# Performance work log

Measured on AMD Instinct MI355X. Metric: run time of the kernel, lower is better.

## Reference

```python
import jax, jax.numpy as jnp
import numpy as np

B, S, D, H = 4, 2048, 1024, 16
DEPTH = D // H  # 64


def setup_inputs() -> dict:
    key = jax.random.key(0)
    ks = jax.random.split(key, 11)
    scale = 1.0 / np.sqrt(D)
    inp = {
        "v": jax.random.normal(ks[0], (B, S, D), jnp.float32),
        "k": jax.random.normal(ks[1], (B, S, D), jnp.float32),
        "q": jax.random.normal(ks[2], (B, S, D), jnp.float32),
        # causal mask: 1.0 where attention is disallowed (strict upper triangle)
        "mask": jnp.triu(jnp.ones((S, S), jnp.float32), k=1)[None, None, :, :],
        "wq": jax.random.normal(ks[3], (D, D), jnp.float32) * scale,
        "bq": jnp.zeros((D,), jnp.float32),
        "wk": jax.random.normal(ks[4], (D, D), jnp.float32) * scale,
        "bk": jnp.zeros((D,), jnp.float32),
        "wv": jax.random.normal(ks[5], (D, D), jnp.float32) * scale,
        "bv": jnp.zeros((D,), jnp.float32),
        "wo": jax.random.normal(ks[6], (D, D), jnp.float32) * scale,
        "bo": jnp.zeros((D,), jnp.float32),
    }
    return inp


def _split_heads(x):
    # [B, S, D] -> [B, H, S, depth]
    b, s, _ = x.shape
    return x.reshape(b, s, H, DEPTH).transpose(0, 2, 1, 3)


def reference(v, k, q, mask, wq, bq, wk, bk, wv, bv, wo, bo):
    qh = _split_heads(q @ wq + bq)  # [B,H,S,depth]
    kh = _split_heads(k @ wk + bk)
    vh = _split_heads(v @ wv + bv)

    logits = jnp.einsum("bhqd,bhkd->bhqk", qh, kh) / jnp.sqrt(
        jnp.asarray(DEPTH, jnp.float32)
    )
    logits = logits + mask * -1e9
    attn = jax.nn.softmax(logits, axis=-1)  # [B,H,S,S]
    out = jnp.einsum("bhqk,bhkd->bhqd", attn, vh)
    out = out.transpose(0, 2, 1, 3).reshape(q.shape[0], -1, D)  # [B,S,D]
    return out @ wo + bo
```

## Files before the change

### kernel.cpp

```cpp
#include <hip/hip_runtime.h>

typedef _Float16 f16;
typedef _Float16 half8 __attribute__((ext_vector_type(8)));
typedef _Float16 half4v __attribute__((ext_vector_type(4)));
typedef _Float16 half2v __attribute__((ext_vector_type(2)));
typedef float f32x4 __attribute__((ext_vector_type(4)));

__device__ __forceinline__ void gl_lds16(const void* g, void* l) {
    __builtin_amdgcn_global_load_lds((const __attribute__((address_space(1))) void*)g,
                                     (__attribute__((address_space(3))) void*)l, 16, 0, 0);
}

__device__ __forceinline__ unsigned pack_f16(float a, float b) {
    union { half2v h; unsigned u; } un;
    un.h[0] = (f16)a; un.h[1] = (f16)b;
    return un.u;
}

__device__ __forceinline__ void prep_w_body(const float* __restrict__ W, f16* __restrict__ Wt)
{
    __shared__ float t[64][65];
    const int tid = threadIdx.x;
    const int tk = blockIdx.x * 64, tn = blockIdx.y * 64;
    const int rr = tid >> 4, cc = (tid & 15) * 4;
    #pragma unroll
    for (int j = 0; j < 4; ++j) {
        float4 v = *(const float4*)(W + (size_t)(tk + rr + j * 16) * 1024 + tn + cc);
        t[rr + j * 16][cc] = v.x; t[rr + j * 16][cc + 1] = v.y;
        t[rr + j * 16][cc + 2] = v.z; t[rr + j * 16][cc + 3] = v.w;
    }
    __syncthreads();
    const int n = tid >> 2, kc = (tid & 3) * 16;
    f16 o[16];
    #pragma unroll
    for (int j = 0; j < 16; ++j) o[j] = (f16)t[kc + j][n];
    f16* dst = Wt + (size_t)(tn + n) * 1024 + tk + kc;
    *(uint4*)dst = *(uint4*)o;
    *(uint4*)(dst + 8) = *(uint4*)(o + 8);
}

__global__ __launch_bounds__(256) void prep_w1(const float* __restrict__ W, f16* __restrict__ Wt)
{ prep_w_body(W, Wt); }

__global__ __launch_bounds__(256) void prep_w3(const float* __restrict__ w0,
    const float* __restrict__ w1, const float* __restrict__ w2, f16* __restrict__ Wt)
{
    const int z = blockIdx.z;
    const float* W = (z == 0) ? w0 : (z == 1) ? w1 : w2;
    prep_w_body(W, Wt + (size_t)z * 1024 * 1024);
}

__global__ __launch_bounds__(512, 4) void qkv_gemm(
    const float* __restrict__ Xq, const float* __restrict__ Xk, const float* __restrict__ Xv,
    const f16* __restrict__ Wt,
    const float* __restrict__ bqp, const float* __restrict__ bkp, const float* __restrict__ bvp,
    f16* __restrict__ qh, f16* __restrict__ kh, f16* __restrict__ vth)
{
    __shared__ __align__(16) f16 As[2][128 * 32];
    __shared__ __align__(16) f16 Bs[2][256 * 32];

    const int z = blockIdx.z;
    const float* X    = (z == 0) ? Xq : (z == 1) ? Xk : Xv;
    const float* bias = (z == 0) ? bqp : (z == 1) ? bkp : bvp;
    const f16*   W    = Wt + (size_t)z * 1024 * 1024;

    const int tid = threadIdx.x;
    const int lane = tid & 63;
    const int lane16 = lane & 15, quad = lane >> 4;
    const int l2 = lane16 & 3;
    const int wave = tid >> 6;
    const int wm = (wave & 1) * 64;
    const int wn = (wave >> 1) * 64;

    const int lin = blockIdx.x + 4 * blockIdx.y;
    const int xcd = lin & 7, t = lin >> 3;
    const int m0 = (((t >> 2) << 3) | xcd) * 128;
    const int n0 = (t & 3) * 256;

    const int xrow = tid >> 2, xch = tid & 3;
    const size_t xgbase = (size_t)(m0 + xrow) * 1024 + xch * 8;
    f16* const pA0 = As[0] + xrow * 32 + ((xch ^ (xrow & 3)) * 8);
    f16* const pA1 = As[1] + xrow * 32 + ((xch ^ (xrow & 3)) * 8);

    const int wrow0 = tid >> 2;
    const int wch = tid & 3;
    const size_t wg0 = (size_t)(n0 + wrow0) * 1024 + ((wch ^ (wrow0 & 3)) * 8);
    const size_t wg1 = (size_t)(n0 + 128 + wrow0) * 1024 + ((wch ^ (wrow0 & 3)) * 8);
    const int wldsbase = (tid & 448) * 8;

    f32x4 acc[4][4] = {};

    {
        float4 x0 = *(const float4*)(X + xgbase);
        float4 x1 = *(const float4*)(X + xgbase + 4);
        gl_lds16(W + wg0, Bs[0] + wldsbase);
        gl_lds16(W + wg1, Bs[0] + 4096 + wldsbase);
        asm volatile("s_waitcnt vmcnt(2)" ::: "memory");
        half8 hx;
        hx[0] = (f16)x0.x; hx[1] = (f16)x0.y; hx[2] = (f16)x0.z; hx[3] = (f16)x0.w;
        hx[4] = (f16)x1.x; hx[5] = (f16)x1.y; hx[6] = (f16)x1.z; hx[7] = (f16)x1.w;
        *(half8*)pA0 = hx;
        asm volatile("s_waitcnt vmcnt(0) lgkmcnt(0)" ::: "memory");
        __builtin_amdgcn_s_barrier();
        asm volatile("" ::: "memory");
    }

    for (int kt = 0; kt < 32; ++kt) {
        const int cur = kt & 1;
        const bool pf = (kt + 1 < 32);
        const f16* Ab = As[cur];
        const f16* Bb = Bs[cur];

        float4 x0, x1;
        if (pf) {
            const int k1 = (kt + 1) * 32;
            x0 = *(const float4*)(X + xgbase + k1);
            x1 = *(const float4*)(X + xgbase + k1 + 4);
            gl_lds16(W + wg0 + k1, Bs[cur ^ 1] + wldsbase);
            gl_lds16(W + wg1 + k1, Bs[cur ^ 1] + 4096 + wldsbase);
        }

        half8 af[4], bf[4];
        #pragma unroll
        for (int i = 0; i < 4; ++i)
            af[i] = *(const half8*)(Ab + (wm + i * 16 + lane16) * 32 + ((quad ^ l2) * 8));
        #pragma unroll
        for (int i = 0; i < 4; ++i)
            bf[i] = *(const half8*)(Bb + (wn + i * 16 + lane16) * 32 + ((quad ^ l2) * 8));
        #pragma unroll
        for (int mi = 0; mi < 4; ++mi)
            #pragma unroll
            for (int ni = 0; ni < 4; ++ni)
                acc[mi][ni] = __builtin_amdgcn_mfma_f32_16x16x32_f16(af[mi], bf[ni], acc[mi][ni], 0, 0, 0);

        if (pf) {
            asm volatile("s_waitcnt vmcnt(2)" ::: "memory");
            half8 hx;
            hx[0] = (f16)x0.x; hx[1] = (f16)x0.y; hx[2] = (f16)x0.z; hx[3] = (f16)x0.w;
            hx[4] = (f16)x1.x; hx[5] = (f16)x1.y; hx[6] = (f16)x1.z; hx[7] = (f16)x1.w;
            *(half8*)((cur == 1) ? pA0 : pA1) = hx;
        }
        asm volatile("s_waitcnt vmcnt(0) lgkmcnt(0)" ::: "memory");
        __builtin_amdgcn_s_barrier();
        asm volatile("" ::: "memory");
    }

    #pragma unroll
    for (int mi = 0; mi < 4; ++mi) {
        #pragma unroll
        for (int ni = 0; ni < 4; ++ni) {
            const int col = n0 + wn + ni * 16 + lane16;
            const float bval = bias[col];
            const int grow0 = m0 + wm + mi * 16 + quad * 4;
            if (z == 2) {
                const int b = grow0 >> 11, s0 = grow0 & 2047;
                const int h = col >> 6, d = col & 63;
                half4v p;
                #pragma unroll
                for (int r = 0; r < 4; ++r) p[r] = (f16)(acc[mi][ni][r] + bval);
                *(half4v*)(vth + (((size_t)b * 16 + h) * 64 + d) * 2048 + s0) = p;
            } else {
                f16* out = (z == 0) ? qh : kh;
                #pragma unroll
                for (int r = 0; r < 4; ++r)
                    out[(size_t)(grow0 + r) * 1024 + col] = (f16)(acc[mi][ni][r] + bval);
            }
        }
    }
}

__global__ __launch_bounds__(256, 2) void out_gemm(
    const f16* __restrict__ X, const f16* __restrict__ Wt,
    const float* __restrict__ bias, float* __restrict__ out)
{
    __shared__ __align__(16) f16 As[2][128 * 64];
    __shared__ __align__(16) f16 Bs[2][128 * 64];

    const int tid = threadIdx.x;
    const int lane = tid & 63;
    const int lane16 = lane & 15, quad = lane >> 4;
    const int wave = tid >> 6;
    const int wm = (wave >> 1) * 64, wn = (wave & 1) * 64;

    const int lin = blockIdx.x + 8 * blockIdx.y;
    const int xcd = lin & 7, t = lin >> 3;
    const int m0 = ((t >> 3) * 8 + xcd) * 128;
    const int n0 = (t & 7) * 128;

    const int wbase = tid & 192;
    const int srow = tid >> 3, schunk = tid & 7;
    const int swc = schunk ^ (srow & 7);

    f32x4 acc[4][4] = {};

    #pragma unroll
    for (int i = 0; i < 4; ++i) {
        gl_lds16(Wt + (size_t)(n0 + i * 32 + srow) * 1024 + swc * 8, Bs[0] + (size_t)(i * 256 + wbase) * 8);
        gl_lds16(X  + (size_t)(m0 + i * 32 + srow) * 1024 + swc * 8, As[0] + (size_t)(i * 256 + wbase) * 8);
    }

    for (int kt = 0; kt < 16; ++kt) {
        if (kt + 1 < 16) {
            const int nb = (kt + 1) & 1;
            const int k1 = (kt + 1) * 64;
            #pragma unroll
            for (int i = 0; i < 4; ++i) {
                gl_lds16(Wt + (size_t)(n0 + i * 32 + srow) * 1024 + k1 + swc * 8, Bs[nb] + (size_t)(i * 256 + wbase) * 8);
                gl_lds16(X  + (size_t)(m0 + i * 32 + srow) * 1024 + k1 + swc * 8, As[nb] + (size_t)(i * 256 + wbase) * 8);
            }
            asm volatile("s_waitcnt vmcnt(8)" ::: "memory");
        } else {
            asm volatile("s_waitcnt vmcnt(0)" ::: "memory");
        }
        __builtin_amdgcn_s_barrier();
        asm volatile("" ::: "memory");

        const f16* Ab = As[kt & 1];
        const f16* Bb = Bs[kt & 1];
        half8 af[4][2], bf[4][2];
        #pragma unroll
        for (int i = 0; i < 4; ++i) {
            const int ra = wm + i * 16 + lane16;
            const int rb = wn + i * 16 + lane16;
            #pragma unroll
            for (int c = 0; c < 2; ++c) {
                af[i][c] = *(const half8*)(Ab + ra * 64 + (((c * 4 + quad) ^ (ra & 7)) * 8));
                bf[i][c] = *(const half8*)(Bb + rb * 64 + (((c * 4 + quad) ^ (rb & 7)) * 8));
            }
        }
        #pragma unroll
        for (int c = 0; c < 2; ++c)
            #pragma unroll
            for (int mi = 0; mi < 4; ++mi)
                #pragma unroll
                for (int ni = 0; ni < 4; ++ni)
                    acc[mi][ni] = __builtin_amdgcn_mfma_f32_16x16x32_f16(af[mi][c], bf[ni][c], acc[mi][ni], 0, 0, 0);

        asm volatile("" ::: "memory");
        __builtin_amdgcn_s_barrier();
        asm volatile("" ::: "memory");
    }

    #pragma unroll
    for (int mi = 0; mi < 4; ++mi) {
        #pragma unroll
        for (int ni = 0; ni < 4; ++ni) {
            const int col = n0 + wn + ni * 16 + lane16;
            const float bval = bias[col];
            const int grow0 = m0 + wm + mi * 16 + quad * 4;
            #pragma unroll
            for (int r = 0; r < 4; ++r)
                out[(size_t)(grow0 + r) * 1024 + col] = acc[mi][ni][r] + bval;
        }
    }
}

__global__ __launch_bounds__(256, 4) void attn_kernel(
    const f16* __restrict__ qh, const f16* __restrict__ kh,
    const f16* __restrict__ vt, f16* __restrict__ at)
{
    __shared__ __align__(16) f16 Ks[2][64 * 64];
    __shared__ __align__(16) f16 Vts[2][64 * 64];

    const int tid = threadIdx.x;
    const int lane = tid & 63, wave = tid >> 6;
    const int lane16 = lane & 15, quad = lane >> 4;
    const int wbase = tid & 192;
    const int l3 = lane16 & 7;
    const int srow = tid >> 3, schunk = tid & 7;

    const int lin = blockIdx.x + 16 * blockIdx.y;
    const int xcd = lin & 7, t = lin >> 3;
    const int bh = xcd + 8 * (t & 7);
    const int qi = 15 - (t >> 3);
    const int b = bh >> 4, h = bh & 15;

    const f16* qp = qh + (size_t)b * 2048 * 1024 + h * 64;
    const f16* kp = kh + (size_t)b * 2048 * 1024 + h * 64;
    const f16* vtp = vt + (size_t)bh * 64 * 2048;

    const int qb = 128 * qi;
    const int qrow0 = qb + wave * 32;
    const int ntiles = qb / 64 + 2;
    const int qmax = qrow0 + 31;

    #pragma unroll
    for (int i = 0; i < 2; ++i) {
        const int row = i * 32 + srow;
        const int sw = (schunk ^ (row & 7)) * 8;
        gl_lds16(kp + (size_t)row * 1024 + sw, Ks[0] + (size_t)(i * 256 + wbase) * 8);
        gl_lds16(vtp + (size_t)row * 2048 + sw, Vts[0] + (size_t)(i * 256 + wbase) * 8);
    }

    half8 aq[2][2];
    #pragma unroll
    for (int mt = 0; mt < 2; ++mt)
        #pragma unroll
        for (int c = 0; c < 2; ++c)
            aq[mt][c] = *(const half8*)(qp + (size_t)(qrow0 + mt * 16 + lane16) * 1024 + c * 32 + quad * 8);

    f32x4 o[4][2] = {};
    float lp[2] = {0.0f, 0.0f};

    for (int kt = 0; kt < ntiles; ++kt) {
        if (kt + 1 < ntiles) {
            const int nb = (kt + 1) & 1;
            const int k1 = (kt + 1) * 64;
            #pragma unroll
            for (int i = 0; i < 2; ++i) {
                const int row = i * 32 + srow;
                const int sw = (schunk ^ (row & 7)) * 8;
                gl_lds16(kp + (size_t)(k1 + row) * 1024 + sw, Ks[nb] + (size_t)(i * 256 + wbase) * 8);
                gl_lds16(vtp + (size_t)row * 2048 + k1 + sw, Vts[nb] + (size_t)(i * 256 + wbase) * 8);
            }
            asm volatile("s_waitcnt vmcnt(4)" ::: "memory");
        } else {
            asm volatile("s_waitcnt vmcnt(0)" ::: "memory");
        }
        __builtin_amdgcn_s_barrier();
        asm volatile("" ::: "memory");

        const int k0 = kt * 64;
        if (k0 <= qmax) {
            const f16* Kb = Ks[kt & 1];
            const f16* Vb = Vts[kt & 1];
            f32x4 sT[4][2];
            #pragma unroll
            for (int sub = 0; sub < 4; ++sub) {
                const int kr = sub * 16 + lane16;
                const half8 ak0 = *(const half8*)(Kb + kr * 64 + ((quad ^ l3) * 8));
                const half8 ak1 = *(const half8*)(Kb + kr * 64 + (((4 + quad) ^ l3) * 8));
                #pragma unroll
                for (int mt = 0; mt < 2; ++mt) {
                    f32x4 z = {};
                    z = __builtin_amdgcn_mfma_f32_16x16x32_f16(ak0, aq[mt][0], z, 0, 0, 0);
                    z = __builtin_amdgcn_mfma_f32_16x16x32_f16(ak1, aq[mt][1], z, 0, 0, 0);
                    sT[sub][mt] = z;
                }
            }
            const bool needmask = (k0 + 63 > qrow0);
            if (needmask) {
                #pragma unroll
                for (int sub = 0; sub < 4; ++sub)
                    #pragma unroll
                    for (int mt = 0; mt < 2; ++mt)
                        #pragma unroll
                        for (int r = 0; r < 4; ++r) {
                            const int key = k0 + sub * 16 + quad * 4 + r;
                            const int qi2 = qrow0 + mt * 16 + lane16;
                            if (key > qi2) sT[sub][mt][r] = -1e30f;
                        }
            }

            half8 bp[2][2];
            #pragma unroll
            for (int mt = 0; mt < 2; ++mt) {
                unsigned pk01[4], pk23[4];
                #pragma unroll
                for (int sub = 0; sub < 4; ++sub) {
                    float p[4];
                    #pragma unroll
                    for (int r = 0; r < 4; ++r) {
                        const float x = fmaf(sT[sub][mt][r], 0.18033688011112042f, -5.770780163555852f);
                        float e;
                        asm("v_exp_f32 %0, %1" : "=v"(e) : "v"(x));
                        p[r] = e;
                        lp[mt] += e;
                    }
                    pk01[sub] = pack_f16(p[0], p[1]);
                    pk23[sub] = pack_f16(p[2], p[3]);
                }
                #pragma unroll
                for (int c = 0; c < 2; ++c) {
                    unsigned a0 = pk01[2 * c], b0 = pk01[2 * c + 1];
                    unsigned a1 = pk23[2 * c], b1 = pk23[2 * c + 1];
                    asm("v_permlane32_swap_b32 %0, %1" : "+v"(a0), "+v"(b0));
                    asm("v_permlane16_swap_b32 %0, %1" : "+v"(a0), "+v"(b0));
                    asm("v_permlane32_swap_b32 %0, %1" : "+v"(a1), "+v"(b1));
                    asm("v_permlane16_swap_b32 %0, %1" : "+v"(a1), "+v"(b1));
                    union { unsigned u[4]; half8 h8; } un;
                    un.u[0] = a0; un.u[1] = a1; un.u[2] = b0; un.u[3] = b1;
                    bp[c][mt] = un.h8;
                }
            }

            #pragma unroll
            for (int nt = 0; nt < 4; ++nt) {
                const int dr = nt * 16 + lane16;
                const half8 av0 = *(const half8*)(Vb + dr * 64 + ((quad ^ l3) * 8));
                const half8 av1 = *(const half8*)(Vb + dr * 64 + (((4 + quad) ^ l3) * 8));
                #pragma unroll
                for (int mt = 0; mt < 2; ++mt) {
                    o[nt][mt] = __builtin_amdgcn_mfma_f32_16x16x32_f16(av0, bp[0][mt], o[nt][mt], 0, 0, 0);
                    o[nt][mt] = __builtin_amdgcn_mfma_f32_16x16x32_f16(av1, bp[1][mt], o[nt][mt], 0, 0, 0);
                }
            }
        }
        asm volatile("" ::: "memory");
        __builtin_amdgcn_s_barrier();
        asm volatile("" ::: "memory");
    }

    #pragma unroll
    for (int mt = 0; mt < 2; ++mt) {
        float red = lp[mt];
        red += __shfl_xor(red, 16);
        red += __shfl_xor(red, 32);
        const float inv = 1.0f / red;
        const int sr = qrow0 + mt * 16 + lane16;
        f16* dst = at + ((size_t)b * 2048 + sr) * 1024 + h * 64 + quad * 4;
        #pragma unroll
        for (int nt = 0; nt < 4; ++nt) {
            half4v p;
            #pragma unroll
            for (int r = 0; r < 4; ++r) p[r] = (f16)(o[nt][mt][r] * inv);
            *(half4v*)(dst + nt * 16) = p;
        }
    }
}

extern "C" void kernel_launch(void* const* d_in, const int* in_sizes, int n_in,
                              void* d_out, int out_size, void* d_ws, size_t ws_size,
                              hipStream_t stream)
{
    const float* v  = (const float*)d_in[0];
    const float* k  = (const float*)d_in[1];
    const float* q  = (const float*)d_in[2];
    const float* wq = (const float*)d_in[4];
    const float* bq = (const float*)d_in[5];
    const float* wk = (const float*)d_in[6];
    const float* bk = (const float*)d_in[7];
    const float* wv = (const float*)d_in[8];
    const float* bv = (const float*)d_in[9];
    const float* wo = (const float*)d_in[10];
    const float* bo = (const float*)d_in[11];

    f16* qh = (f16*)d_ws;
    f16* kh = qh + (size_t)8 * 1024 * 1024;
    f16* vt = kh + (size_t)8 * 1024 * 1024;
    f16* at = vt + (size_t)8 * 1024 * 1024;

    f16* wT = (f16*)d_out;
    f16* woT = qh;

    prep_w3<<<dim3(16, 16, 3), 256, 0, stream>>>(wq, wk, wv, wT);

    qkv_gemm<<<dim3(4, 64, 3), 512, 0, stream>>>(q, k, v, wT, bq, bk, bv, qh, kh, vt);

    attn_kernel<<<dim3(16, 64), 256, 0, stream>>>(qh, kh, vt, at);

    prep_w1<<<dim3(16, 16), 256, 0, stream>>>(wo, woT);
    out_gemm<<<dim3(8, 64), 256, 0, stream>>>(at, woT, bo, (float*)d_out);
}
```

Baseline: 324.7 us.

## Shrink output GEMM tiles and fold Wo transpose into the weight prep launch

The output projection GEMM moves from 128x128 tiles with K-step 64 to 64x128 tiles with K-step 32. It now runs 1024 blocks at higher occupancy, with one wave per 32-column slice. When the workspace is large enough, the Wo transpose is merged into a single four-weight prep launch writing to a separate buffer, which removes one kernel launch and its serialization before out_gemm. The smaller tiles lower per-block reuse and double the number of K iterations and barriers, in exchange for more parallelism and latency hiding.

```diff
diff --git a/kernel.cpp b/kernel.cpp
--- a/kernel.cpp
+++ b/kernel.cpp
@@ -48,6 +48,16 @@
     const int z = blockIdx.z;
     const float* W = (z == 0) ? w0 : (z == 1) ? w1 : w2;
     prep_w_body(W, Wt + (size_t)z * 1024 * 1024);
+}
+
+__global__ __launch_bounds__(256) void prep_w4(const float* __restrict__ w0,
+    const float* __restrict__ w1, const float* __restrict__ w2, const float* __restrict__ w3,
+    f16* __restrict__ Wt, f16* __restrict__ woT)
+{
+    const int z = blockIdx.z;
+    const float* W = (z == 0) ? w0 : (z == 1) ? w1 : (z == 2) ? w2 : w3;
+    f16* dst = (z == 3) ? woT : (Wt + (size_t)z * 1024 * 1024);
+    prep_w_body(W, dst);
 }
 
 __global__ __launch_bounds__(512, 4) void qkv_gemm(
@@ -169,85 +179,79 @@
     }
 }
 
-__global__ __launch_bounds__(256, 2) void out_gemm(
+__global__ __launch_bounds__(256, 4) void out_gemm(
     const f16* __restrict__ X, const f16* __restrict__ Wt,
     const float* __restrict__ bias, float* __restrict__ out)
 {
-    __shared__ __align__(16) f16 As[2][128 * 64];
-    __shared__ __align__(16) f16 Bs[2][128 * 64];
+    __shared__ __align__(16) f16 As[2][64 * 32];
+    __shared__ __align__(16) f16 Bs[2][128 * 32];
 
     const int tid = threadIdx.x;
     const int lane = tid & 63;
     const int lane16 = lane & 15, quad = lane >> 4;
+    const int l2 = lane16 & 3;
     const int wave = tid >> 6;
-    const int wm = (wave >> 1) * 64, wn = (wave & 1) * 64;
+    const int wn = wave * 32;
 
     const int lin = blockIdx.x + 8 * blockIdx.y;
     const int xcd = lin & 7, t = lin >> 3;
-    const int m0 = ((t >> 3) * 8 + xcd) * 128;
+    const int m0 = ((t >> 3) * 8 + xcd) * 64;
     const int n0 = (t & 7) * 128;
 
-    const int wbase = tid & 192;
-    const int srow = tid >> 3, schunk = tid & 7;
-    const int swc = schunk ^ (srow & 7);
-
-    f32x4 acc[4][4] = {};
-
-    #pragma unroll
-    for (int i = 0; i < 4; ++i) {
-        gl_lds16(Wt + (size_t)(n0 + i * 32 + srow) * 1024 + swc * 8, Bs[0] + (size_t)(i * 256 + wbase) * 8);
-        gl_lds16(X  + (size_t)(m0 + i * 32 + srow) * 1024 + swc * 8, As[0] + (size_t)(i * 256 + wbase) * 8);
-    }
-
-    for (int kt = 0; kt < 16; ++kt) {
-        if (kt + 1 < 16) {
-            const int nb = (kt + 1) & 1;
-            const int k1 = (kt + 1) * 64;
-            #pragma unroll
-            for (int i = 0; i < 4; ++i) {
-                gl_lds16(Wt + (size_t)(n0 + i * 32 + srow) * 1024 + k1 + swc * 8, Bs[nb] + (size_t)(i * 256 + wbase) * 8);
-                gl_lds16(X  + (size_t)(m0 + i * 32 + srow) * 1024 + k1 + swc * 8, As[nb] + (size_t)(i * 256 + wbase) * 8);
-            }
-            asm volatile("s_waitcnt vmcnt(8)" ::: "memory");
-        } else {
-            asm volatile("s_waitcnt vmcnt(0)" ::: "memory");
-        }
+    const int srow = tid >> 2, sch = tid & 3;
+    const int swc = sch ^ (srow & 3);
+    const size_t ag = (size_t)(m0 + srow) * 1024 + swc * 8;
+    const size_t bg0 = (size_t)(n0 + srow) * 1024 + swc * 8;
+    const size_t bg1 = (size_t)(n0 + 64 + srow) * 1024 + swc * 8;
+    const int wldsbase = (tid & 192) * 8;
+
+    f32x4 acc[4][2] = {};
+
+    gl_lds16(X + ag, As[0] + wldsbase);
+    gl_lds16(Wt + bg0, Bs[0] + wldsbase);
+    gl_lds16(Wt + bg1, Bs[0] + 2048 + wldsbase);
+    asm volatile("s_waitcnt vmcnt(0)" ::: "memory");
+    __builtin_amdgcn_s_barrier();
+    asm volatile("" ::: "memory");
+
+    for (int kt = 0; kt < 32; ++kt) {
+        const int cur = kt & 1;
+        const bool pf = (kt + 1 < 32);
+        const f16* Ab = As[cur];
+        const f16* Bb = Bs[cur];
+
+        if (pf) {
+            const int k1 = (kt + 1) * 32;
+            gl_lds16(X + ag + k1, As[cur ^ 1] + wldsbase);
+            gl_lds16(Wt + bg0 + k1, Bs[cur ^ 1] + wldsbase);
+            gl_lds16(Wt + bg1 + k1, Bs[cur ^ 1] + 2048 + wldsbase);
+        }
+
+        half8 af[4], bf[2];
+        #pragma unroll
+        for (int i = 0; i < 4; ++i)
+            af[i] = *(const half8*)(Ab + (i * 16 + lane16) * 32 + ((quad ^ l2) * 8));
+        #pragma unroll
+        for (int i = 0; i < 2; ++i)
+            bf[i] = *(const half8*)(Bb + (wn + i * 16 + lane16) * 32 + ((quad ^ l2) * 8));
+        #pragma unroll
+        for (int mi = 0; mi < 4; ++mi)
+            #pragma unroll
+            for (int ni = 0; ni < 2; ++ni)
+                acc[mi][ni] = __builtin_amdgcn_mfma_f32_16x16x32_f16(af[mi], bf[ni], acc[mi][ni], 0, 0, 0);
+
+        asm volatile("s_waitcnt vmcnt(0)" ::: "memory");
         __builtin_amdgcn_s_barrier();
         asm volatile("" ::: "memory");
-
-        const f16* Ab = As[kt & 1];
-        const f16* Bb = Bs[kt & 1];
-        half8 af[4][2], bf[4][2];
-        #pragma unroll
-        for (int i = 0; i < 4; ++i) {
-            const int ra = wm + i * 16 + lane16;
-            const int rb = wn + i * 16 + lane16;
-            #pragma unroll
-            for (int c = 0; c < 2; ++c) {
-                af[i][c] = *(const half8*)(Ab + ra * 64 + (((c * 4 + quad) ^ (ra & 7)) * 8));
-                bf[i][c] = *(const half8*)(Bb + rb * 64 + (((c * 4 + quad) ^ (rb & 7)) * 8));
-            }
-        }
-        #pragma unroll
-        for (int c = 0; c < 2; ++c)
-            #pragma unroll
-            for (int mi = 0; mi < 4; ++mi)
-                #pragma unroll
-                for (int ni = 0; ni < 4; ++ni)
-                    acc[mi][ni] = __builtin_amdgcn_mfma_f32_16x16x32_f16(af[mi][c], bf[ni][c], acc[mi][ni], 0, 0, 0);
-
-        asm volatile("" ::: "memory");
-        __builtin_amdgcn_s_barrier();
-        asm volatile("" ::: "memory");
     }
 
     #pragma unroll
     for (int mi = 0; mi < 4; ++mi) {
         #pragma unroll
-        for (int ni = 0; ni < 4; ++ni) {
+        for (int ni = 0; ni < 2; ++ni) {
             const int col = n0 + wn + ni * 16 + lane16;
             const float bval = bias[col];
-            const int grow0 = m0 + wm + mi * 16 + quad * 4;
+            const int grow0 = m0 + mi * 16 + quad * 4;
             #pragma unroll
             for (int r = 0; r < 4; ++r)
                 out[(size_t)(grow0 + r) * 1024 + col] = acc[mi][ni][r] + bval;
@@ -441,14 +445,21 @@
     f16* at = vt + (size_t)8 * 1024 * 1024;
 
     f16* wT = (f16*)d_out;
-    f16* woT = qh;
-
-    prep_w3<<<dim3(16, 16, 3), 256, 0, stream>>>(wq, wk, wv, wT);
-
-    qkv_gemm<<<dim3(4, 64, 3), 512, 0, stream>>>(q, k, v, wT, bq, bk, bv, qh, kh, vt);
-
-    attn_kernel<<<dim3(16, 64), 256, 0, stream>>>(qh, kh, vt, at);
-
-    prep_w1<<<dim3(16, 16), 256, 0, stream>>>(wo, woT);
-    out_gemm<<<dim3(8, 64), 256, 0, stream>>>(at, woT, bo, (float*)d_out);
-}
+
+    const bool big_ws = ws_size >= (size_t)66 * 1024 * 1024;
+
+    if (big_ws) {
+        f16* woT = at + (size_t)8 * 1024 * 1024;
+        prep_w4<<<dim3(16, 16, 4), 256, 0, stream>>>(wq, wk, wv, wo, wT, woT);
+        qkv_gemm<<<dim3(4, 64, 3), 512, 0, stream>>>(q, k, v, wT, bq, bk, bv, qh, kh, vt);
+        attn_kernel<<<dim3(16, 64), 256, 0, stream>>>(qh, kh, vt, at);
+        out_gemm<<<dim3(8, 128), 256, 0, stream>>>(at, woT, bo, (float*)d_out);
+    } else {
+        f16* woT = qh;
+        prep_w3<<<dim3(16, 16, 3), 256, 0, stream>>>(wq, wk, wv, wT);
+        qkv_gemm<<<dim3(4, 64, 3), 512, 0, stream>>>(q, k, v, wT, bq, bk, bv, qh, kh, vt);
+        attn_kernel<<<dim3(16, 64), 256, 0, stream>>>(qh, kh, vt, at);
+        prep_w1<<<dim3(16, 16), 256, 0, stream>>>(wo, woT);
+        out_gemm<<<dim3(8, 128), 256, 0, stream>>>(at, woT, bo, (float*)d_out);
+    }
+}
```

After: 318.1 us. -2.0%, faster.
